# Kernel optimization log

Hardware: AMD Instinct MI355X
Metric: run time of the kernel (lower is better)

## Reference

```python
import jax, jax.numpy as jnp
import numpy as np

NUM_HEADS = 12
TEMPORAL_RES = 8


def _ln(x, g, b, eps=1e-5):
    mu = jnp.mean(x, axis=-1, keepdims=True)
    var = jnp.mean((x - mu) ** 2, axis=-1, keepdims=True)
    return (x - mu) * jax.lax.rsqrt(var + eps) * g + b


def setup_inputs() -> dict:
    key = jax.random.key(0)
    ks = jax.random.split(key, 8)
    s = 0.02
    d = 768
    inp = {
        'box_tensors': jax.random.uniform(ks[0], (16, 16, 10, 4), dtype=jnp.float32),
        'box_categories': jax.random.normal(ks[1], (16, 10, d), dtype=jnp.float32) * s,
        'w1': jax.random.normal(ks[2], (4, d // 2), dtype=jnp.float32) * s,
        'w2': jax.random.normal(ks[3], (d // 2, d), dtype=jnp.float32) * s,
        'ln1_g': jnp.ones((d,), jnp.float32),
        'ln1_b': jnp.zeros((d,), jnp.float32),
        'wqkv': jax.random.normal(ks[4], (d, 3 * d), dtype=jnp.float32) * s,
        'wo': jax.random.normal(ks[5], (d, d), dtype=jnp.float32) * s,
        'bo': jnp.zeros((d,), jnp.float32),
        'ln2_g': jnp.ones((d,), jnp.float32),
        'ln2_b': jnp.zeros((d,), jnp.float32),
        'wfc1': jax.random.normal(ks[6], (d, 4 * d), dtype=jnp.float32) * s,
        'bfc1': jnp.zeros((4 * d,), jnp.float32),
        'wfc2': jax.random.normal(ks[7], (4 * d, d), dtype=jnp.float32) * s,
        'bfc2': jnp.zeros((d,), jnp.float32),
        'H': 14,
        'W': 14,
    }
    return inp


def _forward(box_tensors, box_categories, w1, w2, ln1_g, ln1_b, wqkv, wo, bo,
             ln2_g, ln2_b, wfc1, bfc1, wfc2, bfc2, H, W):
    B, T, O, _ = box_tensors.shape
    d = box_categories.shape[-1]
    # coord -> feature MLP (no biases), then pos-emb add
    h = jax.nn.relu(box_tensors @ w1)
    x = jax.nn.relu(h @ w2)                      # [B,T,O,d]
    x = x + box_categories[None]                 # broadcast over batch
    L = T * O
    x = x.reshape(B, L, d)
    # --- self-attention block (pre-LN ViT style) ---
    hn = _ln(x, ln1_g, ln1_b)
    qkv = (hn @ wqkv).reshape(B, L, 3, NUM_HEADS, d // NUM_HEADS)
    q, k, v = qkv[:, :, 0], qkv[:, :, 1], qkv[:, :, 2]   # [B,L,h,dh]
    scale = 1.0 / jnp.sqrt(jnp.asarray(d // NUM_HEADS, x.dtype))
    att = jnp.einsum('bqhd,bkhd->bhqk', q, k) * scale
    att = jax.nn.softmax(att, axis=-1)
    o = jnp.einsum('bhqk,bkhd->bqhd', att, v).reshape(B, L, d)
    x = x + (o @ wo + bo)
    hn = _ln(x, ln2_g, ln2_b)
    x = x + (jax.nn.gelu(hn @ wfc1 + bfc1, approximate=False) @ wfc2 + bfc2)
    feats = x.reshape(B, T, O, d)
    # --- box2spatial layout scatter: sum each object's feature into grid cells inside its box ---
    x1 = jnp.minimum(box_tensors[..., 0], box_tensors[..., 2])
    x2 = jnp.maximum(box_tensors[..., 0], box_tensors[..., 2])
    y1 = jnp.minimum(box_tensors[..., 1], box_tensors[..., 3])
    y2 = jnp.maximum(box_tensors[..., 1], box_tensors[..., 3])
    cy = (jnp.arange(H, dtype=x.dtype) + 0.5) / H    # [H]
    cx = (jnp.arange(W, dtype=x.dtype) + 0.5) / W    # [W]
    in_y = (cy[None, None, None, :] >= y1[..., None]) & (cy[None, None, None, :] <= y2[..., None])  # [B,T,O,H]
    in_x = (cx[None, None, None, :] >= x1[..., None]) & (cx[None, None, None, :] <= x2[..., None])  # [B,T,O,W]
    mask = (in_y[..., :, None] & in_x[..., None, :]).astype(x.dtype)  # [B,T,O,H,W]
    grid = jnp.einsum('btohw,btod->bthwd', mask, feats)               # [B,T,H,W,d]
    # temporal avg pooling to TEMPORAL_RES frames
    Tr = T // TEMPORAL_RES
    if Tr > 1:
        grid = grid.reshape(B, T // Tr, Tr, H, W, d).mean(axis=2)
    return grid.reshape(B, -1, d)                 # [B, T'*H*W, d]


def reference(box_tensors, box_categories, w1, w2, ln1_g, ln1_b, wqkv, wo, bo,
              ln2_g, ln2_b, wfc1, bfc1, wfc2, bfc2, H, W):
    return _forward(box_tensors, box_categories, w1, w2, ln1_g, ln1_b, wqkv, wo, bo,
                    ln2_g, ln2_b, wfc1, bfc1, wfc2, bfc2, H, W)
```

## Files before the change

kernel.cpp:

```cpp
#include <hip/hip_runtime.h>
#include <hip/hip_bf16.h>
#include <math.h>


#define BATCH 16
#define TT    16
#define OO    10
#define LL    160
#define BL    2560
#define DD    768
#define NH    12
#define DH    64
#define GH    14
#define GW    14
#define TGRP  8

typedef unsigned short ushort_t;
typedef __attribute__((ext_vector_type(8))) __bf16 bf16x8;
typedef __attribute__((ext_vector_type(4))) float f32x4;

__device__ __forceinline__ ushort_t f2bf(float f) {
    unsigned int u = __float_as_uint(f);
    u += 0x7fffu + ((u >> 16) & 1u);
    return (ushort_t)(u >> 16);
}

__device__ __forceinline__ int swz_xcd(int bid, int nwg) {
    return (bid & 7) * (nwg >> 3) + (bid >> 3);
}

__global__ __launch_bounds__(256)
void transpose_w(const float* __restrict__ W, ushort_t* __restrict__ Wt, int K, int N)
{
    __shared__ float s[32][33];
    const int n0 = blockIdx.x * 32, k0 = blockIdx.y * 32;
    const int tx = threadIdx.x & 31, ty = threadIdx.x >> 5;
#pragma unroll
    for (int r = 0; r < 4; ++r)
        s[ty + r * 8][tx] = W[(size_t)(k0 + ty + r * 8) * N + n0 + tx];
    __syncthreads();
#pragma unroll
    for (int r = 0; r < 4; ++r)
        Wt[(size_t)(n0 + ty + r * 8) * K + k0 + tx] = f2bf(s[tx][ty + r * 8]);
}

__global__ __launch_bounds__(256)
void box_h(const float* __restrict__ box, const float* __restrict__ w1,
           ushort_t* __restrict__ h)
{
    const int idx = blockIdx.x * 256 + threadIdx.x;
    const int r = idx / 384, j = idx - r * 384;
    const float* bx = box + (size_t)r * 4;
    float v = bx[0] * w1[j] + bx[1] * w1[384 + j] +
              bx[2] * w1[768 + j] + bx[3] * w1[1152 + j];
    h[idx] = f2bf(fmaxf(v, 0.f));
}

__global__ __launch_bounds__(256)
void ln_kernel(const float* __restrict__ in, const float* __restrict__ g,
               const float* __restrict__ bvec, ushort_t* __restrict__ out)
{
    const int r = blockIdx.x;
    const int tid = threadIdx.x;
    const float* row = in + (size_t)r * DD;
    float v0 = row[tid], v1 = row[tid + 256], v2 = row[tid + 512];
    float s  = v0 + v1 + v2;
    float s2 = v0 * v0 + v1 * v1 + v2 * v2;
#pragma unroll
    for (int off = 32; off > 0; off >>= 1) {
        s  += __shfl_down(s, off);
        s2 += __shfl_down(s2, off);
    }
    __shared__ float red[8];
    int wave = tid >> 6, lane = tid & 63;
    if (lane == 0) { red[wave] = s; red[wave + 4] = s2; }
    __syncthreads();
    s  = red[0] + red[1] + red[2] + red[3];
    s2 = red[4] + red[5] + red[6] + red[7];
    float mu  = s * (1.f / DD);
    float var = s2 * (1.f / DD) - mu * mu;
    float inv = rsqrtf(var + 1e-5f);
    ushort_t* op = out + (size_t)r * DD;
    op[tid]       = f2bf((v0 - mu) * inv * g[tid]       + bvec[tid]);
    op[tid + 256] = f2bf((v1 - mu) * inv * g[tid + 256] + bvec[tid + 256]);
    op[tid + 512] = f2bf((v2 - mu) * inv * g[tid + 512] + bvec[tid + 512]);
}

#define LOADF(aa, bb, kk)                                                        \
    _Pragma("unroll")                                                            \
    for (int i = 0; i < 4; ++i) {                                                \
        aa[i] = *reinterpret_cast<const bf16x8*>(ap + (size_t)(i * 16) * lda + (kk)); \
        bb[i] = *reinterpret_cast<const bf16x8*>(bp + (size_t)(i * 16) * ldb + (kk)); \
    }
#define MFMA16(aa, bb)                                                           \
    _Pragma("unroll")                                                            \
    for (int i = 0; i < 4; ++i)                                                  \
        _Pragma("unroll")                                                        \
        for (int j = 0; j < 4; ++j)                                              \
            acc[i][j] = __builtin_amdgcn_mfma_f32_16x16x32_bf16(aa[i], bb[j], acc[i][j], 0, 0, 0);

__global__ __launch_bounds__(64)
void gemm_rf(const ushort_t* __restrict__ A, int lda,
             const ushort_t* __restrict__ Bt, int ldb,
             const float* __restrict__ cat,
             float* __restrict__ Cf, int ldc, int K)
{
    const int lane = threadIdx.x;
    const int l16 = lane & 15, quad = lane >> 4;
    const int row0 = blockIdx.y * 64, col0 = blockIdx.x * 64;

    const ushort_t* ap = A  + (size_t)(row0 + l16) * lda + quad * 8;
    const ushort_t* bp = Bt + (size_t)(col0 + l16) * ldb + quad * 8;

    f32x4 acc[4][4];
#pragma unroll
    for (int i = 0; i < 4; ++i)
#pragma unroll
        for (int j = 0; j < 4; ++j) {
            acc[i][j][0] = 0.f; acc[i][j][1] = 0.f;
            acc[i][j][2] = 0.f; acc[i][j][3] = 0.f;
        }

    bf16x8 a0[4], b0[4], a1[4], b1[4];
    LOADF(a0, b0, 0)
    int kt = 0;
    for (; kt + 64 < K; kt += 64) {
        LOADF(a1, b1, kt + 32)
        MFMA16(a0, b0)
        LOADF(a0, b0, kt + 64)
        MFMA16(a1, b1)
    }
    LOADF(a1, b1, kt + 32)
    MFMA16(a0, b0)
    MFMA16(a1, b1)

    const int q4 = quad * 4;
#pragma unroll
    for (int i = 0; i < 4; ++i)
#pragma unroll
        for (int j = 0; j < 4; ++j) {
            const int gcol = col0 + j * 16 + l16;
#pragma unroll
            for (int r = 0; r < 4; ++r) {
                const int grow = row0 + i * 16 + q4 + r;
                const size_t idx = (size_t)grow * ldc + gcol;
                Cf[idx] = fmaxf(acc[i][j][r], 0.f) + cat[(size_t)(grow % LL) * DD + gcol];
            }
        }
}

#define GLL(gp, lp) __builtin_amdgcn_global_load_lds(                       \
    (const __attribute__((address_space(1))) void*)(gp),                     \
    (__attribute__((address_space(3))) void*)(lp), 16, 0, 0)

template <int MODE, int SPLIT>
__global__ __launch_bounds__(256)
void gemm_lds(const ushort_t* __restrict__ A, int lda,
              const ushort_t* __restrict__ Bt, int ldb,
              const float* __restrict__ bias,
              float* __restrict__ Cf, ushort_t* __restrict__ Cb,
              int ldc, int K)
{
    __shared__ ushort_t As[2][8192];
    __shared__ ushort_t Bs[2][8192];

    const int t    = threadIdx.x;
    const int wv   = t >> 6;
    const int lane = t & 63;
    const int l16  = lane & 15, quad = lane >> 4;
    const int wr   = (wv >> 1) * 64;
    const int wc   = (wv & 1) * 64;

    const int nwg = gridDim.x * gridDim.y * gridDim.z;
    const int bid = blockIdx.x + gridDim.x * (blockIdx.y + gridDim.y * blockIdx.z);
    const int w   = swz_xcd(bid, nwg);
    const int bx  = w % gridDim.x;
    const int byz = w / gridDim.x;
    const int by  = byz % gridDim.y;
    const int bz  = byz / gridDim.y;

    const int row0 = by * 128, col0 = bx * 128;
    const int Kper = K / SPLIT;
    const int k0   = bz * Kper;
    const int steps = Kper / 64;

    const ushort_t* Ag = A  + (size_t)(row0 + (t & 127)) * lda + k0 + ((t >> 7) * 8);
    const ushort_t* Bg = Bt + (size_t)(col0 + (t & 127)) * ldb + k0 + ((t >> 7) * 8);

#define STAGE(c, kk) do {                                                    \
        _Pragma("unroll")                                                    \
        for (int ii = 0; ii < 4; ++ii) {                                     \
            GLL(Ag + (kk) + ii * 16, &As[c][ii * 2048 + wv * 512]);          \
            GLL(Bg + (kk) + ii * 16, &Bs[c][ii * 2048 + wv * 512]);          \
        }                                                                    \
    } while (0)

    f32x4 acc[4][4];
#pragma unroll
    for (int i = 0; i < 4; ++i)
#pragma unroll
        for (int j = 0; j < 4; ++j) {
            acc[i][j][0] = 0.f; acc[i][j][1] = 0.f;
            acc[i][j][2] = 0.f; acc[i][j][3] = 0.f;
        }

    STAGE(0, 0);
    __syncthreads();
    int cur = 0;
    for (int s = 0; s < steps; ++s) {
        if (s + 1 < steps) STAGE(cur ^ 1, (s + 1) * 64);
#pragma unroll
        for (int ks = 0; ks < 2; ++ks) {
            bf16x8 af[4], bfr[4];
#pragma unroll
            for (int i = 0; i < 4; ++i)
                af[i] = *reinterpret_cast<const bf16x8*>(
                    &As[cur][((ks * 4 + quad) * 128 + wr + i * 16 + l16) * 8]);
#pragma unroll
            for (int j = 0; j < 4; ++j)
                bfr[j] = *reinterpret_cast<const bf16x8*>(
                    &Bs[cur][((ks * 4 + quad) * 128 + wc + j * 16 + l16) * 8]);
#pragma unroll
            for (int i = 0; i < 4; ++i)
#pragma unroll
                for (int j = 0; j < 4; ++j)
                    acc[i][j] = __builtin_amdgcn_mfma_f32_16x16x32_bf16(
                        af[i], bfr[j], acc[i][j], 0, 0, 0);
        }
        __syncthreads();
        cur ^= 1;
    }
#undef STAGE

    const int q4 = quad * 4;
    const int r0w = row0 + wr, c0w = col0 + wc;
#pragma unroll
    for (int i = 0; i < 4; ++i)
#pragma unroll
        for (int j = 0; j < 4; ++j) {
            const int gcol = c0w + j * 16 + l16;
            const float bj = (MODE == 1 || MODE == 2) ? bias[gcol] : 0.f;
#pragma unroll
            for (int r = 0; r < 4; ++r) {
                const int grow = r0w + i * 16 + q4 + r;
                const size_t idx = (size_t)grow * ldc + gcol;
                const float v = acc[i][j][r];
                if (MODE == 1) {
                    Cf[idx] += v + bj;
                } else if (MODE == 2) {
                    const float u = v + bj;
                    Cb[idx] = f2bf(0.5f * u * (1.f + erff(u * 0.70710678118654752f)));
                } else if (MODE == 3) {
                    Cb[idx] = f2bf(v);
                } else {
                    Cf[(size_t)bz * (BL * DD) + idx] = v;
                }
            }
        }
}

__global__ __launch_bounds__(256)
void reduce_fc2(const float* __restrict__ P, const float* __restrict__ bias,
                float* __restrict__ x)
{
    const int i4 = (blockIdx.x * 256 + threadIdx.x) * 4;
    f32x4 a  = *reinterpret_cast<const f32x4*>(&x[i4]);
    f32x4 p0 = *reinterpret_cast<const f32x4*>(&P[i4]);
    f32x4 p1 = *reinterpret_cast<const f32x4*>(&P[BL * DD + i4]);
    f32x4 b  = *reinterpret_cast<const f32x4*>(&bias[i4 % DD]);
    a = a + p0 + p1 + b;
    *reinterpret_cast<f32x4*>(&x[i4]) = a;
}

#define KS_STRIDE 72
#define VT_STRIDE 168
__global__ __launch_bounds__(320)
void attention_mfma(ushort_t* __restrict__ qkv)
{
    __shared__ ushort_t Ks[160 * KS_STRIDE];
    __shared__ ushort_t Vt[64 * VT_STRIDE];
    __shared__ ushort_t Pb[5][32 * VT_STRIDE];

    const int b  = blockIdx.x / NH;
    const int hh = blockIdx.x % NH;
    ushort_t* basew = qkv + (size_t)b * LL * (3 * DD) + hh * DH;
    const ushort_t* base = basew;
    const int tid  = threadIdx.x;
    const int wave = tid >> 6, lane = tid & 63;
    const int l16 = lane & 15, quad = lane >> 4;

#pragma unroll
    for (int it = 0; it < 4; ++it) {
        int idx = tid + it * 320;
        int l = idx >> 3, c8 = (idx & 7) * 8;
        uint4 kv = *(const uint4*)(base + (size_t)l * (3 * DD) + DD + c8);
        *(uint4*)&Ks[l * KS_STRIDE + c8] = kv;
        uint4 vv = *(const uint4*)(base + (size_t)l * (3 * DD) + 2 * DD + c8);
        ushort_t e[8];
        *(uint4*)e = vv;
#pragma unroll
        for (int i = 0; i < 8; ++i)
            Vt[(c8 + i) * VT_STRIDE + l] = e[i];
    }

    const int q0 = wave * 32;
    bf16x8 qf[2][2];
#pragma unroll
    for (int t = 0; t < 2; ++t)
#pragma unroll
        for (int k = 0; k < 2; ++k)
            qf[t][k] = *reinterpret_cast<const bf16x8*>(
                base + (size_t)(q0 + t * 16 + l16) * (3 * DD) + k * 32 + quad * 8);

    __syncthreads();

    f32x4 S0[10], S1[10];
#pragma unroll
    for (int nt = 0; nt < 10; ++nt) {
        f32x4 z = {0.f, 0.f, 0.f, 0.f};
        const ushort_t* kb = &Ks[(nt * 16 + l16) * KS_STRIDE + quad * 8];
        bf16x8 kf0 = *reinterpret_cast<const bf16x8*>(kb);
        bf16x8 kf1 = *reinterpret_cast<const bf16x8*>(kb + 32);
        f32x4 a0 = __builtin_amdgcn_mfma_f32_16x16x32_bf16(qf[0][0], kf0, z, 0, 0, 0);
        S0[nt]   = __builtin_amdgcn_mfma_f32_16x16x32_bf16(qf[0][1], kf1, a0, 0, 0, 0);
        f32x4 a1 = __builtin_amdgcn_mfma_f32_16x16x32_bf16(qf[1][0], kf0, z, 0, 0, 0);
        S1[nt]   = __builtin_amdgcn_mfma_f32_16x16x32_bf16(qf[1][1], kf1, a1, 0, 0, 0);
    }

#pragma unroll
    for (int t = 0; t < 2; ++t) {
        f32x4* S = t ? S1 : S0;
        float mrow[4] = {-1e30f, -1e30f, -1e30f, -1e30f};
#pragma unroll
        for (int nt = 0; nt < 10; ++nt)
#pragma unroll
            for (int r = 0; r < 4; ++r) {
                S[nt][r] *= 0.125f;
                mrow[r] = fmaxf(mrow[r], S[nt][r]);
            }
#pragma unroll
        for (int r = 0; r < 4; ++r) {
            mrow[r] = fmaxf(mrow[r], __shfl_xor(mrow[r], 1));
            mrow[r] = fmaxf(mrow[r], __shfl_xor(mrow[r], 2));
            mrow[r] = fmaxf(mrow[r], __shfl_xor(mrow[r], 4));
            mrow[r] = fmaxf(mrow[r], __shfl_xor(mrow[r], 8));
        }
        float lsum[4] = {0.f, 0.f, 0.f, 0.f};
#pragma unroll
        for (int nt = 0; nt < 10; ++nt)
#pragma unroll
            for (int r = 0; r < 4; ++r) {
                float e = __expf(S[nt][r] - mrow[r]);
                S[nt][r] = e;
                lsum[r] += e;
            }
#pragma unroll
        for (int r = 0; r < 4; ++r) {
            lsum[r] += __shfl_xor(lsum[r], 1);
            lsum[r] += __shfl_xor(lsum[r], 2);
            lsum[r] += __shfl_xor(lsum[r], 4);
            lsum[r] += __shfl_xor(lsum[r], 8);
            lsum[r] = 1.f / lsum[r];
        }
#pragma unroll
        for (int nt = 0; nt < 10; ++nt)
#pragma unroll
            for (int r = 0; r < 4; ++r)
                Pb[wave][(t * 16 + quad * 4 + r) * VT_STRIDE + nt * 16 + l16] =
                    f2bf(S[nt][r] * lsum[r]);
    }
    asm volatile("s_waitcnt lgkmcnt(0)" ::: "memory");

#pragma unroll
    for (int dt = 0; dt < 4; ++dt) {
        f32x4 o0 = {0.f, 0.f, 0.f, 0.f}, o1 = {0.f, 0.f, 0.f, 0.f};
#pragma unroll
        for (int ks = 0; ks < 5; ++ks) {
            bf16x8 vf = *reinterpret_cast<const bf16x8*>(
                &Vt[(dt * 16 + l16) * VT_STRIDE + ks * 32 + quad * 8]);
            bf16x8 p0 = *reinterpret_cast<const bf16x8*>(
                &Pb[wave][(l16) * VT_STRIDE + ks * 32 + quad * 8]);
            bf16x8 p1 = *reinterpret_cast<const bf16x8*>(
                &Pb[wave][(16 + l16) * VT_STRIDE + ks * 32 + quad * 8]);
            o0 = __builtin_amdgcn_mfma_f32_16x16x32_bf16(vf, p0, o0, 0, 0, 0);
            o1 = __builtin_amdgcn_mfma_f32_16x16x32_bf16(vf, p1, o1, 0, 0, 0);
        }
#pragma unroll
        for (int t = 0; t < 2; ++t) {
            f32x4 o = t ? o1 : o0;
            ushort_t pk[4];
#pragma unroll
            for (int r = 0; r < 4; ++r) pk[r] = f2bf(o[r]);
            ushort_t* dst = basew + (size_t)(q0 + t * 16 + l16) * (3 * DD) +
                            dt * 16 + quad * 4;
            *(uint2*)dst = *(const uint2*)pk;
        }
    }
}

__global__ __launch_bounds__(256)
void mask_grid(const float* __restrict__ box, const float* __restrict__ feats,
               float* __restrict__ out)
{
    const int hw = blockIdx.x;
    const int g  = blockIdx.y;
    const int b  = blockIdx.z;
    const int hh = hw / GW, w = hw % GW;
    const float cy = (hh + 0.5f) / (float)GH;
    const float cx = (w  + 0.5f) / (float)GW;
    const int tid = threadIdx.x;

    __shared__ float flg[20];
    if (tid < 20) {
        int t = g * 2 + tid / OO, o = tid % OO;
        const float* bx = box + (size_t)((b * TT + t) * OO + o) * 4;
        float x1 = fminf(bx[0], bx[2]), x2 = fmaxf(bx[0], bx[2]);
        float y1 = fminf(bx[1], bx[3]), y2 = fmaxf(bx[1], bx[3]);
        flg[tid] = (cy >= y1 && cy <= y2 && cx >= x1 && cx <= x2) ? 1.f : 0.f;
    }
    __syncthreads();

    float a0 = 0.f, a1 = 0.f, a2 = 0.f;
#pragma unroll
    for (int p = 0; p < 20; ++p) {
        if (flg[p] != 0.f) {
            int r = (b * TT + g * 2 + p / OO) * OO + (p % OO);
            const float* f = feats + (size_t)r * DD;
            a0 += f[tid]; a1 += f[tid + 256]; a2 += f[tid + 512];
        }
    }
    float* op = out + ((size_t)b * (TGRP * GH * GW) + g * (GH * GW) + hw) * DD;
    op[tid]       = a0 * 0.5f;
    op[tid + 256] = a1 * 0.5f;
    op[tid + 512] = a2 * 0.5f;
}

extern "C" void kernel_launch(void* const* d_in, const int* in_sizes, int n_in,
                              void* d_out, int out_size, void* d_ws, size_t ws_size,
                              hipStream_t stream)
{
    const float* box  = (const float*)d_in[0];
    const float* cat  = (const float*)d_in[1];
    const float* w1   = (const float*)d_in[2];
    const float* w2   = (const float*)d_in[3];
    const float* ln1g = (const float*)d_in[4];
    const float* ln1b = (const float*)d_in[5];
    const float* wqkv = (const float*)d_in[6];
    const float* wo   = (const float*)d_in[7];
    const float* bo   = (const float*)d_in[8];
    const float* ln2g = (const float*)d_in[9];
    const float* ln2b = (const float*)d_in[10];
    const float* wfc1 = (const float*)d_in[11];
    const float* bfc1 = (const float*)d_in[12];
    const float* wfc2 = (const float*)d_in[13];
    const float* bfc2 = (const float*)d_in[14];
    float* out = (float*)d_out;

    char* wsb = (char*)d_ws;
    float*    x     = (float*)   (wsb + 0);
    ushort_t* qkvb  = (ushort_t*)(wsb + 7864320);
    ushort_t* fc1b  = qkvb;
    ushort_t* wfc2T = (ushort_t*)(wsb + 23592960);
    ushort_t* hnb   = (ushort_t*)(wsb + 28311552);
    ushort_t* wqkvT = (ushort_t*)(wsb + 32243712);
    ushort_t* woT   = (ushort_t*)(wsb + 35782656);
    ushort_t* wfc1T = (ushort_t*)(wsb + 36962304);
    ushort_t* w2T   = (ushort_t*)(wsb + 41680896);
    ushort_t* h     = (ushort_t*)(wsb + 42270720);
    float*    fc2P  = (float*)   (wsb + 28311552);

    transpose_w<<<dim3(2304 / 32, 768 / 32), 256, 0, stream>>>(wqkv, wqkvT, 768, 2304);
    transpose_w<<<dim3(768 / 32, 768 / 32), 256, 0, stream>>>(wo, woT, 768, 768);
    transpose_w<<<dim3(3072 / 32, 768 / 32), 256, 0, stream>>>(wfc1, wfc1T, 768, 3072);
    transpose_w<<<dim3(768 / 32, 3072 / 32), 256, 0, stream>>>(wfc2, wfc2T, 3072, 768);
    transpose_w<<<dim3(768 / 32, 384 / 32), 256, 0, stream>>>(w2, w2T, 384, 768);

    box_h<<<BL * 384 / 256, 256, 0, stream>>>(box, w1, h);
    gemm_rf<<<dim3(12, 40, 1), 64, 0, stream>>>(h, 384, w2T, 384, cat, x, DD, 384);
    ln_kernel<<<BL, 256, 0, stream>>>(x, ln1g, ln1b, hnb);
    gemm_lds<3, 1><<<dim3(2304 / 128, 2560 / 128, 1), 256, 0, stream>>>(
        hnb, DD, wqkvT, DD, nullptr, nullptr, qkvb, 3 * DD, DD);
    attention_mfma<<<BATCH * NH, 320, 0, stream>>>(qkvb);
    gemm_lds<1, 1><<<dim3(768 / 128, 2560 / 128, 1), 256, 0, stream>>>(
        qkvb, 3 * DD, woT, DD, bo, x, nullptr, DD, DD);
    ln_kernel<<<BL, 256, 0, stream>>>(x, ln2g, ln2b, hnb);
    gemm_lds<2, 1><<<dim3(3072 / 128, 2560 / 128, 1), 256, 0, stream>>>(
        hnb, DD, wfc1T, DD, bfc1, nullptr, fc1b, 4 * DD, DD);
    gemm_lds<5, 2><<<dim3(768 / 128, 2560 / 128, 2), 256, 0, stream>>>(
        fc1b, 4 * DD, wfc2T, 4 * DD, nullptr, fc2P, nullptr, DD, 4 * DD);
    reduce_fc2<<<BL * DD / 4 / 256, 256, 0, stream>>>(fc2P, bfc2, x);
    mask_grid<<<dim3(GH * GW, TGRP, BATCH), 256, 0, stream>>>(box, x, out);
}
```

Measured before the change: 348.0 us.

## Split-K the out-projection with atomics and use register-file GEMM for fc2

The attention out-projection GEMM is split along K into two slices that accumulate into the residual with atomicAdd, adding the bias only from the first slice, which doubles the number of workgroups for a small grid. The fc2 split-K GEMM moves from the LDS-tiled 128x128 kernel to a new single-wave register-file kernel with 64x64 tiles, giving more, smaller workgroups. The aim is better CU occupancy on these narrow-N GEMMs. The trade-offs are atomic traffic and nondeterministic summation order in the residual, and no LDS reuse in fc2.

New measurement: 344.5 us. Within noise of the previous version (-1.0%).

```diff
diff --git a/kernel.cpp b/kernel.cpp
--- a/kernel.cpp
+++ b/kernel.cpp
@@ -149,6 +149,65 @@
         }
 }
 
+__global__ __launch_bounds__(64)
+void gemm_rf_fc2(const ushort_t* __restrict__ A, int lda,
+                 const ushort_t* __restrict__ Bt, int ldb,
+                 float* __restrict__ P, int ldc, int Kper)
+{
+    const int lane = threadIdx.x;
+    const int l16 = lane & 15, quad = lane >> 4;
+
+    const int nwg = gridDim.x * gridDim.y * gridDim.z;
+    const int bid = blockIdx.x + gridDim.x * (blockIdx.y + gridDim.y * blockIdx.z);
+    const int w   = swz_xcd(bid, nwg);
+    const int bx  = w % gridDim.x;
+    const int byz = w / gridDim.x;
+    const int by  = byz % gridDim.y;
+    const int bz  = byz / gridDim.y;
+
+    const int row0 = by * 64, col0 = bx * 64;
+    const int k0   = bz * Kper;
+
+    const ushort_t* ap = A  + (size_t)(row0 + l16) * lda + k0 + quad * 8;
+    const ushort_t* bp = Bt + (size_t)(col0 + l16) * ldb + k0 + quad * 8;
+
+    f32x4 acc[4][4];
+#pragma unroll
+    for (int i = 0; i < 4; ++i)
+#pragma unroll
+        for (int j = 0; j < 4; ++j) {
+            acc[i][j][0] = 0.f; acc[i][j][1] = 0.f;
+            acc[i][j][2] = 0.f; acc[i][j][3] = 0.f;
+        }
+
+    bf16x8 a0[4], b0[4], a1[4], b1[4];
+    LOADF(a0, b0, 0)
+    int kt = 0;
+    for (; kt + 64 < Kper; kt += 64) {
+        LOADF(a1, b1, kt + 32)
+        MFMA16(a0, b0)
+        LOADF(a0, b0, kt + 64)
+        MFMA16(a1, b1)
+    }
+    LOADF(a1, b1, kt + 32)
+    MFMA16(a0, b0)
+    MFMA16(a1, b1)
+
+    const int q4 = quad * 4;
+    float* Pz = P + (size_t)bz * (BL * DD);
+#pragma unroll
+    for (int i = 0; i < 4; ++i)
+#pragma unroll
+        for (int j = 0; j < 4; ++j) {
+            const int gcol = col0 + j * 16 + l16;
+#pragma unroll
+            for (int r = 0; r < 4; ++r) {
+                const int grow = row0 + i * 16 + q4 + r;
+                Pz[(size_t)grow * ldc + gcol] = acc[i][j][r];
+            }
+        }
+}
+
 #define GLL(gp, lp) __builtin_amdgcn_global_load_lds(                       \
     (const __attribute__((address_space(1))) void*)(gp),                     \
     (__attribute__((address_space(3))) void*)(lp), 16, 0, 0)
@@ -239,21 +298,22 @@
 #pragma unroll
         for (int j = 0; j < 4; ++j) {
             const int gcol = c0w + j * 16 + l16;
-            const float bj = (MODE == 1 || MODE == 2) ? bias[gcol] : 0.f;
+            const float bj = (MODE == 1 || MODE == 2)
+                               ? ((SPLIT == 1 || bz == 0) ? bias[gcol] : 0.f)
+                               : 0.f;
 #pragma unroll
             for (int r = 0; r < 4; ++r) {
                 const int grow = r0w + i * 16 + q4 + r;
                 const size_t idx = (size_t)grow * ldc + gcol;
                 const float v = acc[i][j][r];
                 if (MODE == 1) {
-                    Cf[idx] += v + bj;
+                    if (SPLIT > 1) atomicAdd(&Cf[idx], v + bj);
+                    else           Cf[idx] += v + bj;
                 } else if (MODE == 2) {
                     const float u = v + bj;
                     Cb[idx] = f2bf(0.5f * u * (1.f + erff(u * 0.70710678118654752f)));
-                } else if (MODE == 3) {
+                } else {
                     Cb[idx] = f2bf(v);
-                } else {
-                    Cf[(size_t)bz * (BL * DD) + idx] = v;
                 }
             }
         }
@@ -481,13 +541,13 @@
     gemm_lds<3, 1><<<dim3(2304 / 128, 2560 / 128, 1), 256, 0, stream>>>(
         hnb, DD, wqkvT, DD, nullptr, nullptr, qkvb, 3 * DD, DD);
     attention_mfma<<<BATCH * NH, 320, 0, stream>>>(qkvb);
-    gemm_lds<1, 1><<<dim3(768 / 128, 2560 / 128, 1), 256, 0, stream>>>(
+    gemm_lds<1, 2><<<dim3(768 / 128, 2560 / 128, 2), 256, 0, stream>>>(
         qkvb, 3 * DD, woT, DD, bo, x, nullptr, DD, DD);
     ln_kernel<<<BL, 256, 0, stream>>>(x, ln2g, ln2b, hnb);
     gemm_lds<2, 1><<<dim3(3072 / 128, 2560 / 128, 1), 256, 0, stream>>>(
         hnb, DD, wfc1T, DD, bfc1, nullptr, fc1b, 4 * DD, DD);
-    gemm_lds<5, 2><<<dim3(768 / 128, 2560 / 128, 2), 256, 0, stream>>>(
-        fc1b, 4 * DD, wfc2T, 4 * DD, nullptr, fc2P, nullptr, DD, 4 * DD);
+    gemm_rf_fc2<<<dim3(768 / 64, 2560 / 64, 2), 64, 0, stream>>>(
+        fc1b, 4 * DD, wfc2T, 4 * DD, fc2P, DD, 2 * DD);
     reduce_fc2<<<BL * DD / 4 / 256, 256, 0, stream>>>(fc2P, bfc2, x);
     mask_grid<<<dim3(GH * GW, TGRP, BATCH), 256, 0, stream>>>(box, x, out);
 }
```
